# Performance work log

Hardware: AMD Instinct MI355X
Metric: run time of the kernel (lower is better)

## Reference

```python
import jax, jax.numpy as jnp
import numpy as np

EPS = 1e-5

def _layernorm(x, gamma, beta):
    mu = jnp.mean(x, axis=-1, keepdims=True)
    var = jnp.var(x, axis=-1, keepdims=True)
    return (x - mu) * jax.lax.rsqrt(var + EPS) * gamma + beta

def setup_inputs() -> dict:
    key = jax.random.key(0)
    ks = jax.random.split(key, 6)
    bs, t, dim = 4, 2048, 1024
    x = jax.random.normal(ks[0], (bs, t, dim), dtype=jnp.float32)
    # shared LayerNorm params (same module applied twice in forward)
    ln_gamma = jnp.ones((dim,), dtype=jnp.float32)
    ln_beta = jnp.zeros((dim,), dtype=jnp.float32)
    # Linear params, stored as (in, out)
    w1 = jax.random.normal(ks[1], (dim, 2 * dim), dtype=jnp.float32) / np.sqrt(dim)
    b1 = jax.random.normal(ks[2], (2 * dim,), dtype=jnp.float32) * 0.01
    w2 = jax.random.normal(ks[3], (2 * dim, dim), dtype=jnp.float32) / np.sqrt(2 * dim)
    b2 = jax.random.normal(ks[4], (dim,), dtype=jnp.float32) * 0.01
    return {"x": x, "ln_gamma": ln_gamma, "ln_beta": ln_beta,
            "w1": w1, "b1": b1, "w2": w2, "b2": b2}

def reference(x, ln_gamma, ln_beta, w1, b1, w2, b2):
    # x: [bs, t, f]
    y = _layernorm(x, ln_gamma, ln_beta)
    y = jax.nn.gelu(jnp.einsum('btf,fh->bth', y, w1) + b1, approximate=False)
    y = jnp.einsum('bth,hf->btf', y, w2) + b2
    # attention-like quadratic mix (no softmax): (x @ x^T) @ y
    scores = jnp.einsum('btf,bsf->bts', x, x)          # [bs, t, t]
    y = jnp.einsum('bts,bsf->btf', scores, y)
    y = x + y
    y = _layernorm(y, ln_gamma, ln_beta)
    return y
```

## Files before the change

### kernel.cpp

```cpp
#include <hip/hip_runtime.h>
#include <hip/hip_fp16.h>

typedef _Float16 f16;
typedef _Float16 f16x8 __attribute__((ext_vector_type(8)));
typedef _Float16 f16x4 __attribute__((ext_vector_type(4)));
typedef float f32x4 __attribute__((ext_vector_type(4)));

#define LN_EPS 1e-5f

__device__ __forceinline__ float erf_fast(float x) {
    const float ax = __builtin_fabsf(x);
    const float t = 1.0f / (1.0f + 0.3275911f * ax);
    const float y = t * (0.254829592f +
                    t * (-0.284496736f +
                    t * (1.421413741f +
                    t * (-1.453152027f +
                    t * 1.061405429f))));
    const float r = 1.0f - y * __expf(-ax * ax);
    return __builtin_copysignf(r, x);
}

__device__ __forceinline__ float gelu_exact(float v) {
    return 0.5f * v * (1.0f + erf_fast(v * 0.70710678118654752440f));
}

__device__ __forceinline__ void gload_lds16(const f16* g, f16* l) {
    __builtin_amdgcn_global_load_lds(
        (const __attribute__((address_space(1))) unsigned int*)(g),
        (__attribute__((address_space(3))) unsigned int*)(l),
        16, 0, 0);
}

__global__ __launch_bounds__(256)
void ln_cast_kernel(const float* __restrict__ x,
                    const float* __restrict__ gamma,
                    const float* __restrict__ beta,
                    f16* __restrict__ y_h,
                    f16* __restrict__ x_h) {
    const int row = blockIdx.x;
    const int t = threadIdx.x;
    const size_t base = (size_t)row * 1024;
    float4 v = ((const float4*)(x + base))[t];
    float s  = v.x + v.y + v.z + v.w;
    float s2 = v.x*v.x + v.y*v.y + v.z*v.z + v.w*v.w;
    #pragma unroll
    for (int off = 32; off > 0; off >>= 1) {
        s  += __shfl_down(s, off, 64);
        s2 += __shfl_down(s2, off, 64);
    }
    __shared__ float ls[4], ls2[4];
    const int wid = t >> 6;
    if ((t & 63) == 0) { ls[wid] = s; ls2[wid] = s2; }
    __syncthreads();
    if (t == 0) {
        ls[0]  = ls[0] + ls[1] + ls[2] + ls[3];
        ls2[0] = ls2[0] + ls2[1] + ls2[2] + ls2[3];
    }
    __syncthreads();
    const float mu   = ls[0] * (1.0f / 1024.0f);
    const float var  = ls2[0] * (1.0f / 1024.0f) - mu * mu;
    const float rstd = rsqrtf(var + LN_EPS);
    const float4 g  = ((const float4*)gamma)[t];
    const float4 bt = ((const float4*)beta)[t];
    f16x4 yo, xo;
    yo[0] = (f16)((v.x - mu) * rstd * g.x + bt.x);
    yo[1] = (f16)((v.y - mu) * rstd * g.y + bt.y);
    yo[2] = (f16)((v.z - mu) * rstd * g.z + bt.z);
    yo[3] = (f16)((v.w - mu) * rstd * g.w + bt.w);
    xo[0] = (f16)v.x; xo[1] = (f16)v.y; xo[2] = (f16)v.z; xo[3] = (f16)v.w;
    *(f16x4*)(y_h + base + t * 4) = yo;
    *(f16x4*)(x_h + base + t * 4) = xo;
}

__global__ __launch_bounds__(256)
void ln_final_kernel(const float* __restrict__ pre,
                     const float* __restrict__ gamma,
                     const float* __restrict__ beta,
                     float* __restrict__ out) {
    const int row = blockIdx.x;
    const int t = threadIdx.x;
    const size_t base = (size_t)row * 1024;
    float4 v = ((const float4*)(pre + base))[t];
    float s  = v.x + v.y + v.z + v.w;
    float s2 = v.x*v.x + v.y*v.y + v.z*v.z + v.w*v.w;
    #pragma unroll
    for (int off = 32; off > 0; off >>= 1) {
        s  += __shfl_down(s, off, 64);
        s2 += __shfl_down(s2, off, 64);
    }
    __shared__ float ls[4], ls2[4];
    const int wid = t >> 6;
    if ((t & 63) == 0) { ls[wid] = s; ls2[wid] = s2; }
    __syncthreads();
    if (t == 0) {
        ls[0]  = ls[0] + ls[1] + ls[2] + ls[3];
        ls2[0] = ls2[0] + ls2[1] + ls2[2] + ls2[3];
    }
    __syncthreads();
    const float mu   = ls[0] * (1.0f / 1024.0f);
    const float var  = ls2[0] * (1.0f / 1024.0f) - mu * mu;
    const float rstd = rsqrtf(var + LN_EPS);
    const float4 g  = ((const float4*)gamma)[t];
    const float4 bt = ((const float4*)beta)[t];
    float4 o;
    o.x = (v.x - mu) * rstd * g.x + bt.x;
    o.y = (v.y - mu) * rstd * g.y + bt.y;
    o.z = (v.z - mu) * rstd * g.z + bt.z;
    o.w = (v.w - mu) * rstd * g.w + bt.w;
    ((float4*)(out + base))[t] = o;
}

__global__ __launch_bounds__(256)
void transpose_cast_kernel(const float* __restrict__ src,
                           f16* __restrict__ dst, int R, int C) {
    __shared__ float tile[32][33];
    const int c0 = blockIdx.x * 32, r0 = blockIdx.y * 32;
    const int tx = threadIdx.x & 31, ty = threadIdx.x >> 5;
    #pragma unroll
    for (int i = 0; i < 4; ++i) {
        const int r = ty + i * 8;
        tile[r][tx] = src[(size_t)(r0 + r) * C + c0 + tx];
    }
    __syncthreads();
    #pragma unroll
    for (int i = 0; i < 4; ++i) {
        const int r = ty + i * 8;
        dst[(size_t)(c0 + r) * R + r0 + tx] = (f16)tile[tx][r];
    }
}

__global__ __launch_bounds__(256)
void transpose_f16_kernel(const f16* __restrict__ src,
                          f16* __restrict__ dst, int R, int C) {
    __shared__ f16 tile[32][33];
    const size_t zb = (size_t)blockIdx.z * R * C;
    src += zb; dst += zb;
    const int c0 = blockIdx.x * 32, r0 = blockIdx.y * 32;
    const int tx = threadIdx.x & 31, ty = threadIdx.x >> 5;
    #pragma unroll
    for (int i = 0; i < 4; ++i) {
        const int r = ty + i * 8;
        tile[r][tx] = src[(size_t)(r0 + r) * C + c0 + tx];
    }
    __syncthreads();
    #pragma unroll
    for (int i = 0; i < 4; ++i) {
        const int r = ty + i * 8;
        dst[(size_t)(c0 + r) * R + r0 + tx] = tile[tx][r];
    }
}

template <int EPI>
__global__ __launch_bounds__(256, 3)
void gemm_nt_kernel(const f16* __restrict__ A, const f16* __restrict__ Bt,
                    const float* __restrict__ bias,
                    const float* __restrict__ xadd,
                    f16* __restrict__ outH, float* __restrict__ outF,
                    int M, int N, int K,
                    long long batchA, long long batchB, long long batchC) {
    __shared__ __attribute__((aligned(16))) f16 sA[3][128 * 32];
    __shared__ __attribute__((aligned(16))) f16 sB[3][128 * 32];

    const int z = blockIdx.z;
    A  += (size_t)z * batchA;
    Bt += (size_t)z * batchB;

    const int m0 = blockIdx.x * 128;
    const int n0 = blockIdx.y * 128;
    const int t = threadIdx.x;
    const int l = t & 63;
    const int wid = t >> 6;
    const int wm = (wid >> 1) * 64;
    const int wn = (wid & 1) * 64;

    f32x4 acc[4][4] = {};

    const int rl = l & 15;
    const int ko = (l >> 4) * 8;
    const int nk = K >> 5;

    const int c0 = t, c1 = t + 256;
    const f16* Ag0 = A  + (size_t)(m0 + (c0 >> 2)) * K + (c0 & 3) * 8;
    const f16* Ag1 = A  + (size_t)(m0 + (c1 >> 2)) * K + (c1 & 3) * 8;
    const f16* Bg0 = Bt + (size_t)(n0 + (c0 >> 2)) * K + (c0 & 3) * 8;
    const f16* Bg1 = Bt + (size_t)(n0 + (c1 >> 2)) * K + (c1 & 3) * 8;
    const int lo0 = wid * 512;
    const int lo1 = 2048 + wid * 512;

    gload_lds16(Ag0,      sA[0] + lo0);
    gload_lds16(Ag1,      sA[0] + lo1);
    gload_lds16(Bg0,      sB[0] + lo0);
    gload_lds16(Bg1,      sB[0] + lo1);
    gload_lds16(Ag0 + 32, sA[1] + lo0);
    gload_lds16(Ag1 + 32, sA[1] + lo1);
    gload_lds16(Bg0 + 32, sB[1] + lo0);
    gload_lds16(Bg1 + 32, sB[1] + lo1);

    f16 *curA = sA[0], *nxtA = sA[1], *farA = sA[2];
    f16 *curB = sB[0], *nxtB = sB[1], *farB = sB[2];

    for (int kt = 0; kt < nk; ++kt) {
        asm volatile("s_waitcnt vmcnt(4)" ::: "memory");
        __builtin_amdgcn_s_barrier();

        const int ktn = (kt + 2 < nk) ? kt + 2 : nk - 1;
        const int kof = ktn * 32;
        gload_lds16(Ag0 + kof, farA + lo0);
        gload_lds16(Ag1 + kof, farA + lo1);
        gload_lds16(Bg0 + kof, farB + lo0);
        gload_lds16(Bg1 + kof, farB + lo1);

        f16x8 a[4], b[4];
        #pragma unroll
        for (int f = 0; f < 4; ++f) {
            a[f] = *(const f16x8*)&curA[(wm + f * 16 + rl) * 32 + ko];
            b[f] = *(const f16x8*)&curB[(wn + f * 16 + rl) * 32 + ko];
        }
        #pragma unroll
        for (int fm = 0; fm < 4; ++fm)
            #pragma unroll
            for (int fn = 0; fn < 4; ++fn)
                acc[fm][fn] = __builtin_amdgcn_mfma_f32_16x16x32_f16(
                    a[fm], b[fn], acc[fm][fn], 0, 0, 0);

        f16* tA = curA; curA = nxtA; nxtA = farA; farA = tA;
        f16* tB = curB; curB = nxtB; nxtB = farB; farB = tB;
    }
    asm volatile("s_waitcnt vmcnt(0)" ::: "memory");

    const int rh = l >> 4;
    const float* xaddz = xadd;
    f16* outHz = outH;
    float* outFz = outF;
    if (EPI == 3) {
        outFz += (size_t)z * batchC;
        xaddz += (size_t)z * batchC;
    } else if (EPI == 2) {
        outHz += (size_t)z * batchC;
    }
    #pragma unroll
    for (int fm = 0; fm < 4; ++fm) {
        #pragma unroll
        for (int fn = 0; fn < 4; ++fn) {
            const int col = n0 + wn + fn * 16 + rl;
            if (EPI == 1) {
                const int row0 = m0 + wm + fm * 16 + rh * 4;
                const int zz = row0 >> 11;
                const int rr = row0 & 2047;
                const float bv = bias[col];
                f16x4 o;
                #pragma unroll
                for (int r = 0; r < 4; ++r) o[r] = (f16)(acc[fm][fn][r] + bv);
                *(f16x4*)(outH + ((size_t)zz * N + col) * 2048 + rr) = o;
            } else {
                #pragma unroll
                for (int r = 0; r < 4; ++r) {
                    const int row = m0 + wm + fm * 16 + rh * 4 + r;
                    float v = acc[fm][fn][r];
                    const size_t idx = (size_t)row * N + col;
                    if (EPI == 0) {
                        v += bias[col];
                        outHz[idx] = (f16)gelu_exact(v);
                    } else if (EPI == 2) {
                        outHz[idx] = (f16)v;
                    } else {
                        outFz[idx] = v + xaddz[idx];
                    }
                }
            }
        }
    }
}

extern "C" void kernel_launch(void* const* d_in, const int* in_sizes, int n_in,
                              void* d_out, int out_size, void* d_ws, size_t ws_size,
                              hipStream_t stream) {
    const float* x     = (const float*)d_in[0];
    const float* gamma = (const float*)d_in[1];
    const float* beta  = (const float*)d_in[2];
    const float* w1    = (const float*)d_in[3];
    const float* b1    = (const float*)d_in[4];
    const float* w2    = (const float*)d_in[5];
    const float* b2    = (const float*)d_in[6];
    float* out = (float*)d_out;

    const int BS = 4, T = 2048, DIM = 1024, HID = 2048;
    const int M = BS * T;
    const long long MB = 1024 * 1024;

    char* ws = (char*)d_ws;
    f16*   x_h  = (f16*)(ws + 0 * MB);
    f16*   y_h  = (f16*)(ws + 16 * MB);
    f16*   h    = (f16*)(ws + 32 * MB);
    float* pre  = (float*)h;
    f16*   y2t  = (f16*)(ws + 64 * MB);
    f16*   x_t  = (f16*)(ws + 80 * MB);
    f16*   G    = (f16*)(ws + 96 * MB);
    f16*   w1t  = (f16*)(ws + 104 * MB);
    f16*   w2t  = (f16*)(ws + 108 * MB);

    ln_cast_kernel<<<M, 256, 0, stream>>>(x, gamma, beta, y_h, x_h);

    transpose_cast_kernel<<<dim3(HID / 32, DIM / 32), 256, 0, stream>>>(w1, w1t, DIM, HID);
    transpose_cast_kernel<<<dim3(DIM / 32, HID / 32), 256, 0, stream>>>(w2, w2t, HID, DIM);

    gemm_nt_kernel<0><<<dim3(M / 128, HID / 128, 1), 256, 0, stream>>>(
        y_h, w1t, b1, nullptr, h, nullptr, M, HID, DIM, 0, 0, 0);

    gemm_nt_kernel<1><<<dim3(M / 128, DIM / 128, 1), 256, 0, stream>>>(
        h, w2t, b2, nullptr, y2t, nullptr, M, DIM, HID, 0, 0, 0);

    transpose_f16_kernel<<<dim3(DIM / 32, T / 32, BS), 256, 0, stream>>>(x_h, x_t, T, DIM);

    gemm_nt_kernel<2><<<dim3(DIM / 128, DIM / 128, BS), 256, 0, stream>>>(
        y2t, x_t, nullptr, nullptr, G, nullptr, DIM, DIM, T,
        (long long)DIM * T, (long long)DIM * T, (long long)DIM * DIM);

    gemm_nt_kernel<3><<<dim3(T / 128, DIM / 128, BS), 256, 0, stream>>>(
        x_h, G, nullptr, x, nullptr, pre, T, DIM, DIM,
        (long long)T * DIM, (long long)DIM * DIM, (long long)T * DIM);

    ln_final_kernel<<<M, 256, 0, stream>>>(pre, gamma, beta, out);
}
```

Measured before the change: 226.2 us.

## Add 256x256 eight-wave GEMM with swizzled LDS for first MLP layer

Adds a new 256x256-tile, 512-thread GEMM kernel with a BK=64 XOR-swizzled LDS layout, double buffering, interleaved staging and MFMA phases, and s_setprio hints. It is used for the first linear layer with the GELU epilogue. The existing 128x128 GEMM also gets an XOR swizzle on its LDS layout to reduce bank conflicts on fragment reads. The larger tile raises data reuse but uses about 128KB of LDS and launches fewer blocks (32x8), which may leave some CUs idle.

```diff
diff --git a/kernel.cpp b/kernel.cpp
--- a/kernel.cpp
+++ b/kernel.cpp
@@ -151,6 +151,173 @@
 }
 
 template <int EPI>
+__global__ __launch_bounds__(512, 2)
+void gemm256_nt_kernel(const f16* __restrict__ A, const f16* __restrict__ Bt,
+                       const float* __restrict__ bias, f16* __restrict__ outH,
+                       int M, int N, int K) {
+    __shared__ __attribute__((aligned(16))) f16 sAbuf[2][256 * 64];
+    __shared__ __attribute__((aligned(16))) f16 sBbuf[2][256 * 64];
+
+    const int m0 = blockIdx.x * 256;
+    const int n0 = blockIdx.y * 256;
+    const int t = threadIdx.x;
+    const int l = t & 63;
+    const int wid = t >> 6;
+    const int wr = wid >> 2;
+    const int wc = wid & 3;
+    const int rl = l & 15;
+    const int g  = l >> 4;
+    const int nk = K >> 6;
+
+    const int rowS = wid * 16 + (l >> 3);
+    const int kbS  = ((l & 7) ^ ((l >> 3) & 7)) * 8;
+    const f16* pA = A  + (size_t)(m0 + rowS) * K + kbS;
+    const f16* pB = Bt + (size_t)(n0 + rowS) * K + kbS;
+    const int ldsS = wid * 1024;
+
+    const int rA = wr * 128 + rl;
+    const int rB = wc * 64 + rl;
+    const int swk0 = ((g)     ^ (rl & 7)) * 8;
+    const int swk1 = ((4 + g) ^ (rl & 7)) * 8;
+
+    f32x4 acc[8][4] = {};
+
+    const long long hstep = (long long)128 * K;
+
+    auto stgA = [&](f16* dst, int h, int kc) {
+        const f16* s = pA + (size_t)h * hstep + kc * 64;
+        f16* d = dst + h * 8192 + ldsS;
+        gload_lds16(s, d);
+        gload_lds16(s + 8 * K, d + 512);
+    };
+    auto stgB = [&](f16* dst, int h, int kc) {
+        const f16* s = pB + (size_t)h * hstep + kc * 64;
+        f16* d = dst + h * 8192 + ldsS;
+        gload_lds16(s, d);
+        gload_lds16(s + 8 * K, d + 512);
+    };
+
+    f16* bufA0 = sAbuf[0]; f16* bufA1 = sAbuf[1];
+    f16* bufB0 = sBbuf[0]; f16* bufB1 = sBbuf[1];
+
+    const int t1 = (nk > 1) ? 1 : 0;
+    stgA(bufA0, 0, 0); stgA(bufA0, 1, 0);
+    stgB(bufB0, 0, 0); stgB(bufB0, 1, 0);
+    stgB(bufB1, 0, t1); stgB(bufB1, 1, t1);
+    stgA(bufA1, 0, t1);
+    asm volatile("s_waitcnt vmcnt(6)" ::: "memory");
+    __builtin_amdgcn_s_barrier();
+
+    f16 *Ac = bufA0, *Ao = bufA1, *Bc = bufB0, *Bo = bufB1;
+
+    f16x8 a[4][2], b0r[2][2], b1r[2][2];
+
+    for (int kt = 0; kt < nk; ++kt) {
+        const int kt1 = (kt + 1 < nk) ? kt + 1 : nk - 1;
+        const int kt2 = (kt + 2 < nk) ? kt + 2 : nk - 1;
+
+        #pragma unroll
+        for (int fm = 0; fm < 4; ++fm) {
+            a[fm][0] = *(const f16x8*)(Ac + (rA + fm * 16) * 64 + swk0);
+            a[fm][1] = *(const f16x8*)(Ac + (rA + fm * 16) * 64 + swk1);
+        }
+        #pragma unroll
+        for (int fn = 0; fn < 2; ++fn) {
+            b0r[fn][0] = *(const f16x8*)(Bc + (rB + fn * 16) * 64 + swk0);
+            b0r[fn][1] = *(const f16x8*)(Bc + (rB + fn * 16) * 64 + swk1);
+        }
+        stgA(Ao, 1, kt1);
+        __builtin_amdgcn_s_barrier();
+        asm volatile("s_waitcnt lgkmcnt(0)" ::: "memory");
+        __builtin_amdgcn_sched_barrier(0);
+        __builtin_amdgcn_s_setprio(1);
+        #pragma unroll
+        for (int fm = 0; fm < 4; ++fm)
+            #pragma unroll
+            for (int fn = 0; fn < 2; ++fn) {
+                acc[fm][fn] = __builtin_amdgcn_mfma_f32_16x16x32_f16(a[fm][0], b0r[fn][0], acc[fm][fn], 0, 0, 0);
+                acc[fm][fn] = __builtin_amdgcn_mfma_f32_16x16x32_f16(a[fm][1], b0r[fn][1], acc[fm][fn], 0, 0, 0);
+            }
+        __builtin_amdgcn_s_setprio(0);
+        __builtin_amdgcn_s_barrier();
+
+        #pragma unroll
+        for (int fn = 0; fn < 2; ++fn) {
+            b1r[fn][0] = *(const f16x8*)(Bc + (rB + (fn + 2) * 16) * 64 + swk0);
+            b1r[fn][1] = *(const f16x8*)(Bc + (rB + (fn + 2) * 16) * 64 + swk1);
+        }
+        __builtin_amdgcn_s_barrier();
+        asm volatile("s_waitcnt lgkmcnt(0)" ::: "memory");
+        __builtin_amdgcn_sched_barrier(0);
+        __builtin_amdgcn_s_setprio(1);
+        #pragma unroll
+        for (int fm = 0; fm < 4; ++fm)
+            #pragma unroll
+            for (int fn = 0; fn < 2; ++fn) {
+                acc[fm][fn + 2] = __builtin_amdgcn_mfma_f32_16x16x32_f16(a[fm][0], b1r[fn][0], acc[fm][fn + 2], 0, 0, 0);
+                acc[fm][fn + 2] = __builtin_amdgcn_mfma_f32_16x16x32_f16(a[fm][1], b1r[fn][1], acc[fm][fn + 2], 0, 0, 0);
+            }
+        __builtin_amdgcn_s_setprio(0);
+        __builtin_amdgcn_s_barrier();
+
+        #pragma unroll
+        for (int fm = 0; fm < 4; ++fm) {
+            a[fm][0] = *(const f16x8*)(Ac + (rA + (fm + 4) * 16) * 64 + swk0);
+            a[fm][1] = *(const f16x8*)(Ac + (rA + (fm + 4) * 16) * 64 + swk1);
+        }
+        stgB(Bc, 0, kt2);
+        __builtin_amdgcn_s_barrier();
+        asm volatile("s_waitcnt lgkmcnt(0)" ::: "memory");
+        __builtin_amdgcn_sched_barrier(0);
+        __builtin_amdgcn_s_setprio(1);
+        #pragma unroll
+        for (int fm = 0; fm < 4; ++fm)
+            #pragma unroll
+            for (int fn = 0; fn < 2; ++fn) {
+                acc[fm + 4][fn + 2] = __builtin_amdgcn_mfma_f32_16x16x32_f16(a[fm][0], b1r[fn][0], acc[fm + 4][fn + 2], 0, 0, 0);
+                acc[fm + 4][fn + 2] = __builtin_amdgcn_mfma_f32_16x16x32_f16(a[fm][1], b1r[fn][1], acc[fm + 4][fn + 2], 0, 0, 0);
+            }
+        __builtin_amdgcn_s_setprio(0);
+        __builtin_amdgcn_s_barrier();
+
+        stgB(Bc, 1, kt2);
+        stgA(Ac, 0, kt2);
+        __builtin_amdgcn_s_barrier();
+        __builtin_amdgcn_s_setprio(1);
+        #pragma unroll
+        for (int fm = 0; fm < 4; ++fm)
+            #pragma unroll
+            for (int fn = 0; fn < 2; ++fn) {
+                acc[fm + 4][fn] = __builtin_amdgcn_mfma_f32_16x16x32_f16(a[fm][0], b0r[fn][0], acc[fm + 4][fn], 0, 0, 0);
+                acc[fm + 4][fn] = __builtin_amdgcn_mfma_f32_16x16x32_f16(a[fm][1], b0r[fn][1], acc[fm + 4][fn], 0, 0, 0);
+            }
+        __builtin_amdgcn_s_setprio(0);
+        asm volatile("s_waitcnt vmcnt(6)" ::: "memory");
+        __builtin_amdgcn_s_barrier();
+
+        f16* tp;
+        tp = Ac; Ac = Ao; Ao = tp;
+        tp = Bc; Bc = Bo; Bo = tp;
+    }
+    asm volatile("s_waitcnt vmcnt(0)" ::: "memory");
+
+    #pragma unroll
+    for (int fm = 0; fm < 8; ++fm) {
+        #pragma unroll
+        for (int fn = 0; fn < 4; ++fn) {
+            const int col = n0 + wc * 64 + fn * 16 + rl;
+            const float bv = bias[col];
+            #pragma unroll
+            for (int r = 0; r < 4; ++r) {
+                const int row = m0 + wr * 128 + fm * 16 + g * 4 + r;
+                const float v = acc[fm][fn][r] + bv;
+                outH[(size_t)row * N + col] = (f16)gelu_exact(v);
+            }
+        }
+    }
+}
+
+template <int EPI>
 __global__ __launch_bounds__(256, 3)
 void gemm_nt_kernel(const f16* __restrict__ A, const f16* __restrict__ Bt,
                     const float* __restrict__ bias,
@@ -176,16 +343,18 @@
     f32x4 acc[4][4] = {};
 
     const int rl = l & 15;
-    const int ko = (l >> 4) * 8;
     const int nk = K >> 5;
 
-    const int c0 = t, c1 = t + 256;
-    const f16* Ag0 = A  + (size_t)(m0 + (c0 >> 2)) * K + (c0 & 3) * 8;
-    const f16* Ag1 = A  + (size_t)(m0 + (c1 >> 2)) * K + (c1 & 3) * 8;
-    const f16* Bg0 = Bt + (size_t)(n0 + (c0 >> 2)) * K + (c0 & 3) * 8;
-    const f16* Bg1 = Bt + (size_t)(n0 + (c1 >> 2)) * K + (c1 & 3) * 8;
+    const int row0 = t >> 2;
+    const int kb = ((t & 3) ^ (row0 & 3)) * 8;
+    const f16* Ag0 = A  + (size_t)(m0 + row0) * K + kb;
+    const f16* Ag1 = A  + (size_t)(m0 + row0 + 64) * K + kb;
+    const f16* Bg0 = Bt + (size_t)(n0 + row0) * K + kb;
+    const f16* Bg1 = Bt + (size_t)(n0 + row0 + 64) * K + kb;
     const int lo0 = wid * 512;
     const int lo1 = 2048 + wid * 512;
+
+    const int swk = (((l >> 4) ^ (rl & 3))) * 8;
 
     gload_lds16(Ag0,      sA[0] + lo0);
     gload_lds16(Ag1,      sA[0] + lo1);
@@ -213,8 +382,8 @@
         f16x8 a[4], b[4];
         #pragma unroll
         for (int f = 0; f < 4; ++f) {
-            a[f] = *(const f16x8*)&curA[(wm + f * 16 + rl) * 32 + ko];
-            b[f] = *(const f16x8*)&curB[(wn + f * 16 + rl) * 32 + ko];
+            a[f] = *(const f16x8*)&curA[(wm + f * 16 + rl) * 32 + swk];
+            b[f] = *(const f16x8*)&curB[(wn + f * 16 + rl) * 32 + swk];
         }
         #pragma unroll
         for (int fm = 0; fm < 4; ++fm)
@@ -244,9 +413,9 @@
         for (int fn = 0; fn < 4; ++fn) {
             const int col = n0 + wn + fn * 16 + rl;
             if (EPI == 1) {
-                const int row0 = m0 + wm + fm * 16 + rh * 4;
-                const int zz = row0 >> 11;
-                const int rr = row0 & 2047;
+                const int row0o = m0 + wm + fm * 16 + rh * 4;
+                const int zz = row0o >> 11;
+                const int rr = row0o & 2047;
                 const float bv = bias[col];
                 f16x4 o;
                 #pragma unroll
@@ -258,10 +427,7 @@
                     const int row = m0 + wm + fm * 16 + rh * 4 + r;
                     float v = acc[fm][fn][r];
                     const size_t idx = (size_t)row * N + col;
-                    if (EPI == 0) {
-                        v += bias[col];
-                        outHz[idx] = (f16)gelu_exact(v);
-                    } else if (EPI == 2) {
+                    if (EPI == 2) {
                         outHz[idx] = (f16)v;
                     } else {
                         outFz[idx] = v + xaddz[idx];
@@ -304,8 +470,8 @@
     transpose_cast_kernel<<<dim3(HID / 32, DIM / 32), 256, 0, stream>>>(w1, w1t, DIM, HID);
     transpose_cast_kernel<<<dim3(DIM / 32, HID / 32), 256, 0, stream>>>(w2, w2t, HID, DIM);
 
-    gemm_nt_kernel<0><<<dim3(M / 128, HID / 128, 1), 256, 0, stream>>>(
-        y_h, w1t, b1, nullptr, h, nullptr, M, HID, DIM, 0, 0, 0);
+    gemm256_nt_kernel<0><<<dim3(M / 256, HID / 256), 512, 0, stream>>>(
+        y_h, w1t, b1, h, M, HID, DIM);
 
     gemm_nt_kernel<1><<<dim3(M / 128, DIM / 128, 1), 256, 0, stream>>>(
         h, w2t, b2, nullptr, y2t, nullptr, M, DIM, HID, 0, 0, 0);
```

New measurement: 212.2 us. 1.07x faster.
